# Kernel tuning notes

Hardware: AMD Instinct MI355X
Metric: run time of the kernel (lower is better)

## Reference

```python
import jax, jax.numpy as jnp
import numpy as np

HIDDEN = 2048
HEADS = 16
HEAD_DIM = HIDDEN // HEADS  # 128
THETA = 10000.0


def _rope_cache(seq_len, dim, theta=THETA):
    inv_freq = 1.0 / (theta ** (jnp.arange(0, dim, 2, dtype=jnp.float32) / dim))
    t = jnp.arange(seq_len, dtype=jnp.float32)
    freqs = jnp.outer(t, inv_freq)            # [S, dim/2]
    emb = jnp.concatenate([freqs, freqs], -1)  # [S, dim]
    return jnp.cos(emb), jnp.sin(emb)


def _rotate_half(x):
    x1, x2 = jnp.split(x, 2, axis=-1)
    return jnp.concatenate([-x2, x1], axis=-1)


def setup_inputs() -> dict:
    key = jax.random.key(0)
    ks = jax.random.split(key, 5)
    B, S = 2, 2048
    scale = 1.0 / np.sqrt(HIDDEN)
    return {
        "hidden_states": jax.random.normal(ks[0], (B, S, HIDDEN), jnp.float32),
        "wq": jax.random.normal(ks[1], (HIDDEN, HIDDEN), jnp.float32) * scale,
        "wk": jax.random.normal(ks[2], (HIDDEN, HIDDEN), jnp.float32) * scale,
        "wv": jax.random.normal(ks[3], (HIDDEN, HIDDEN), jnp.float32) * scale,
        "wo": jax.random.normal(ks[4], (HIDDEN, HIDDEN), jnp.float32) * scale,
    }


def reference(hidden_states, wq, wk, wv, wo):
    B, S, D = hidden_states.shape
    H, Hd = HEADS, HEAD_DIM
    # projections (nn.Linear: x @ W^T), reshape to [B, H, S, Hd]
    def proj(w):
        return (hidden_states @ w.T).reshape(B, S, H, Hd).transpose(0, 2, 1, 3)
    q, k, v = proj(wq), proj(wk), proj(wv)
    # RoPE
    cos, sin = _rope_cache(S, Hd)             # [S, Hd]
    q = q * cos + _rotate_half(q) * sin
    k = k * cos + _rotate_half(k) * sin
    # scaled dot-product attention with causal mask
    scores = jnp.einsum("bhqd,bhkd->bhqk", q, k) / jnp.sqrt(jnp.float32(Hd))
    causal = jnp.tril(jnp.ones((S, S), bool))
    scores = jnp.where(causal, scores, -jnp.inf)
    attn = jax.nn.softmax(scores, axis=-1)
    out = jnp.einsum("bhqk,bhkd->bhqd", attn, v)  # [B, H, S, Hd]
    out = out.transpose(0, 2, 1, 3).reshape(B, S, D)
    return out @ wo.T
```

## Files before the change

### kernel.cpp

```cpp
#include <hip/hip_runtime.h>
#include <hip/hip_bf16.h>

#define S_LEN  2048
#define BATCH  2
#define NH     16
#define HD     128
#define HIDDEN 2048
#define MROWS  (BATCH*S_LEN)

typedef __attribute__((ext_vector_type(8))) short bf16x8;
typedef __attribute__((ext_vector_type(4))) short s16x4;
typedef __attribute__((ext_vector_type(4))) float f32x4;

__device__ __forceinline__ float bf2f(short s) {
    union { float f; unsigned int u; } v;
    v.u = ((unsigned int)(unsigned short)s) << 16;
    return v.f;
}
__device__ __forceinline__ short f2bf(float f) {
    union { float f; unsigned int u; } v;
    v.f = f;
    unsigned int r = v.u + 0x7fffu + ((v.u >> 16) & 1u);
    return (short)(r >> 16);
}
__device__ __forceinline__ f32x4 mfma16(bf16x8 a, bf16x8 b, f32x4 c) {
    return __builtin_amdgcn_mfma_f32_16x16x32_bf16(a, b, c, 0, 0, 0);
}
__device__ __forceinline__ void gload16(const void* g, void* l) {
    __builtin_amdgcn_global_load_lds(
        (const __attribute__((address_space(1))) void*)g,
        (__attribute__((address_space(3))) void*)l, 16, 0, 0);
}

#define SEG (4194304)
__global__ void cast_k(const float* hs, const float* wq, const float* wk,
                       const float* wv, const float* wo, short* dst)
{
    size_t i = ((size_t)blockIdx.x * 256 + threadIdx.x) * 8;
    int seg = (int)(i >> 22);
    const float* s;
    size_t off;
    if (seg < 2)      { s = hs; off = i; }
    else if (seg == 2){ s = wq; off = i - 2 * (size_t)SEG; }
    else if (seg == 3){ s = wk; off = i - 3 * (size_t)SEG; }
    else if (seg == 4){ s = wv; off = i - 4 * (size_t)SEG; }
    else              { s = wo; off = i - 5 * (size_t)SEG; }
    f32x4 lo = *(const f32x4*)(s + off);
    f32x4 hi = *(const f32x4*)(s + off + 4);
    short v[8];
#pragma unroll
    for (int j = 0; j < 4; ++j) { v[j] = f2bf(lo[j]); v[4 + j] = f2bf(hi[j]); }
    *(bf16x8*)(dst + i) = *(bf16x8*)v;
}

template<int MODE>
__global__ __launch_bounds__(256, 4)
void gemm_bt(const short* A, const short* W0, const short* W1, const short* W2,
             short* Oq, short* Ok, short* Ov, float* Of)
{
    __shared__ short smem[2 * 128 * 64];
    short* As = smem;
    short* Bs = smem + 128 * 64;

    const int tid  = threadIdx.x;
    const int lane = tid & 63;
    const int wv   = tid >> 6;
    const int wr   = wv >> 1, wc = wv & 1;
    const int fr   = lane & 15, fg = lane >> 4;

    const int mt = blockIdx.x;
    int nt = blockIdx.y;
    const short* W = W0;
    short* Ob = Oq;
    int osel = 0;
    if (MODE == 0) {
        osel = nt >> 4; nt &= 15;
        W  = (osel == 0) ? W0 : (osel == 1) ? W1 : W2;
        Ob = (osel == 0) ? Oq : (osel == 1) ? Ok : Ov;
    }
    const int row0 = mt * 128, col0 = nt * 128;
    const int sr = tid >> 3, sb = tid & 7;

    f32x4 acc[4][4];
#pragma unroll
    for (int m = 0; m < 4; ++m)
#pragma unroll
        for (int n = 0; n < 4; ++n) acc[m][n] = (f32x4){0.f, 0.f, 0.f, 0.f};

    for (int k0 = 0; k0 < HIDDEN; k0 += 64) {
        __syncthreads();
#pragma unroll
        for (int it = 0; it < 4; ++it) {
            int r = it * 32 + sr;
            gload16(A + (size_t)(row0 + r) * HIDDEN + k0 + ((sb ^ (r & 7)) * 8),
                    (char*)As + (it * 256 + wv * 64) * 16);
        }
#pragma unroll
        for (int it = 0; it < 4; ++it) {
            int r = it * 32 + sr;
            gload16(W + (size_t)(col0 + r) * HIDDEN + k0 + ((sb ^ (r & 7)) * 8),
                    (char*)Bs + (it * 256 + wv * 64) * 16);
        }
        __syncthreads();
#pragma unroll
        for (int ks = 0; ks < 2; ++ks) {
            bf16x8 a[4], b[4];
#pragma unroll
            for (int m = 0; m < 4; ++m) {
                int r = wr * 64 + m * 16 + fr;
                a[m] = *(const bf16x8*)&As[r * 64 + (((ks * 4 + fg) ^ (r & 7)) * 8)];
            }
#pragma unroll
            for (int n = 0; n < 4; ++n) {
                int r = wc * 64 + n * 16 + fr;
                b[n] = *(const bf16x8*)&Bs[r * 64 + (((ks * 4 + fg) ^ (r & 7)) * 8)];
            }
#pragma unroll
            for (int m = 0; m < 4; ++m)
#pragma unroll
                for (int n = 0; n < 4; ++n)
                    acc[m][n] = mfma16(a[m], b[n], acc[m][n]);
        }
    }

    if (MODE == 0 && osel == 2) {
        __syncthreads();
#pragma unroll
        for (int m = 0; m < 4; ++m)
#pragma unroll
            for (int j = 0; j < 4; ++j) {
                int row = wr * 64 + m * 16 + fg * 4 + j;
#pragma unroll
                for (int n = 0; n < 4; ++n) {
                    int col = wc * 64 + n * 16 + fr;
                    smem[col * 128 + (((row >> 3) ^ (col & 15)) * 8) + (row & 7)] =
                        f2bf(acc[m][n][j]);
                }
            }
        __syncthreads();
        const int b_ = row0 >> 11;
        const int bh = b_ * NH + nt;
        const int s0 = row0 & (S_LEN - 1);
#pragma unroll
        for (int it = 0; it < 8; ++it) {
            int c = it * 256 + tid;
            int d = c >> 4, sbk = c & 15;
            bf16x8 vv = *(const bf16x8*)&smem[d * 128 + ((sbk ^ (d & 15)) * 8)];
            *(bf16x8*)(Ov + ((size_t)bh * HD + d) * S_LEN + s0 + sbk * 8) = vv;
        }
    } else {
#pragma unroll
        for (int m = 0; m < 4; ++m)
#pragma unroll
            for (int j = 0; j < 4; ++j) {
                int mrow = row0 + wr * 64 + m * 16 + fg * 4 + j;
#pragma unroll
                for (int n = 0; n < 4; ++n) {
                    int col = col0 + wc * 64 + n * 16 + fr;
                    float val = acc[m][n][j];
                    if (MODE == 0) {
                        int b_ = mrow >> 11, s = mrow & (S_LEN - 1);
                        int h = col >> 7, d = col & (HD - 1);
                        Ob[((size_t)(b_ * NH + h) * S_LEN + s) * HD + d] = f2bf(val);
                    } else {
                        Of[(size_t)mrow * HIDDEN + col] = val;
                    }
                }
            }
    }
}

__global__ void rope_table_k(float* tab)
{
    int i = blockIdx.x * 256 + threadIdx.x;
    if (i >= S_LEN * 64) return;
    int s = i >> 6, d = i & 63;
    float inv = 1.0f / powf(10000.0f, (float)d * (1.0f / 64.0f));
    float ang = (float)s * inv;
    tab[2 * i]     = cosf(ang);
    tab[2 * i + 1] = sinf(ang);
}

__global__ void rope_apply_k(short* Q, short* K, const float* tab)
{
    int i = blockIdx.x * 256 + threadIdx.x;
    int d8 = i & 7;
    int s  = (i >> 3) & (S_LEN - 1);
    int bh = i >> 14;
    size_t base = ((size_t)bh * S_LEN + s) * HD + d8 * 8;
    const float* tp = tab + (s * 64 + d8 * 8) * 2;
    f32x4 t[4];
#pragma unroll
    for (int j = 0; j < 4; ++j) t[j] = *(const f32x4*)(tp + j * 4);

    bf16x8 q1 = *(bf16x8*)(Q + base), q2 = *(bf16x8*)(Q + base + 64);
    bf16x8 k1 = *(bf16x8*)(K + base), k2 = *(bf16x8*)(K + base + 64);
    short oq1[8], oq2[8], ok1[8], ok2[8];
    const float qs = 0.08838834764831845f;
#pragma unroll
    for (int j = 0; j < 8; ++j) {
        float c  = t[j >> 1][(j & 1) * 2];
        float sn = t[j >> 1][(j & 1) * 2 + 1];
        float a1 = bf2f(q1[j]), a2 = bf2f(q2[j]);
        oq1[j] = f2bf((a1 * c - a2 * sn) * qs);
        oq2[j] = f2bf((a2 * c + a1 * sn) * qs);
        float b1 = bf2f(k1[j]), b2 = bf2f(k2[j]);
        ok1[j] = f2bf(b1 * c - b2 * sn);
        ok2[j] = f2bf(b2 * c + b1 * sn);
    }
    *(bf16x8*)(Q + base)      = *(bf16x8*)oq1;
    *(bf16x8*)(Q + base + 64) = *(bf16x8*)oq2;
    *(bf16x8*)(K + base)      = *(bf16x8*)ok1;
    *(bf16x8*)(K + base + 64) = *(bf16x8*)ok2;
}

__global__ __launch_bounds__(256, 2)
void attn_k(const short* Q, const short* K, const short* Vt, short* AO)
{
    __shared__ short Ks[2][64 * 128];
    __shared__ short Vs[2][128 * 64];

    const int tid = threadIdx.x, lane = tid & 63, wv = tid >> 6;
    const int fr = lane & 15, fg = lane >> 4;
    const int bid = blockIdx.x;
    const int bh   = bid & 31;
    const int sub  = bid >> 5;
    const int p    = sub >> 1;
    const int half = sub & 1;

    const short* Qb = Q  + (size_t)bh * S_LEN * HD;
    const short* Kb = K  + (size_t)bh * S_LEN * HD;
    const short* Vb = Vt + (size_t)bh * HD * S_LEN;
    const int b_ = bh >> 4, h = bh & 15;

#define SWK(r) (((r) & 3) | ((((r) >> 3) & 3) << 2))
#define STAGE(t, bufi)                                                          \
    do {                                                                        \
        const int kb_ = (t) * 64;                                               \
        _Pragma("unroll")                                                       \
        for (int i_ = 0; i_ < 4; ++i_) {                                        \
            int c_ = i_ * 256 + tid;                                            \
            int r_ = c_ >> 4, bb_ = c_ & 15;                                    \
            gload16(Kb + (size_t)(kb_ + r_) * HD + ((bb_ ^ SWK(r_)) * 8),       \
                    (char*)&Ks[bufi][0] + (i_ * 256 + wv * 64) * 16);           \
        }                                                                       \
        _Pragma("unroll")                                                       \
        for (int i_ = 0; i_ < 4; ++i_) {                                        \
            int c_ = i_ * 256 + tid;                                            \
            int r_ = c_ >> 3, bb_ = c_ & 7;                                     \
            gload16(Vb + (size_t)r_ * S_LEN + kb_ + ((bb_ ^ (r_ & 7)) * 8),     \
                    (char*)&Vs[bufi][0] + (i_ * 256 + wv * 64) * 16);           \
        }                                                                       \
    } while (0)

#pragma unroll 1
    for (int phase = 0; phase < 2; ++phase) {
        const int qt = phase ? (15 - p) : p;
        const int qbase = qt * 128 + half * 64 + wv * 16;

        bf16x8 qf[4];
#pragma unroll
        for (int ks = 0; ks < 4; ++ks)
            qf[ks] = *(const bf16x8*)(Qb + (size_t)(qbase + fr) * HD
                                      + ks * 32 + fg * 8);

        f32x4 oT[8];
#pragma unroll
        for (int nd = 0; nd < 8; ++nd) oT[nd] = (f32x4){0.f, 0.f, 0.f, 0.f};
        float mrun = -1e30f, lrun = 0.f;

        const int ntiles = qt * 2 + 1 + half;
        __syncthreads();
        STAGE(0, 0);

        for (int t = 0; t < ntiles; ++t) {
            const int buf = t & 1;
            __syncthreads();
            if (t + 1 < ntiles) STAGE(t + 1, buf ^ 1);
            const int kb = t * 64;

            if (kb <= qbase + 15) {
                f32x4 sc[4];
#pragma unroll
                for (int ni = 0; ni < 4; ++ni) sc[ni] = (f32x4){0.f, 0.f, 0.f, 0.f};
                __builtin_amdgcn_s_setprio(1);
#pragma unroll
                for (int ks = 0; ks < 4; ++ks) {
                    bf16x8 kf[4];
#pragma unroll
                    for (int ni = 0; ni < 4; ++ni) {
                        int rk = ((ni & 1) << 5) + ((fr >> 2) << 3)
                               + ((ni >> 1) << 2) + (fr & 3);
                        kf[ni] = *(const bf16x8*)&Ks[buf][rk * 128
                                     + (((ks * 4 + fg) ^ fr) * 8)];
                    }
#pragma unroll
                    for (int ni = 0; ni < 4; ++ni)
                        sc[ni] = mfma16(kf[ni], qf[ks], sc[ni]);
                }
                __builtin_amdgcn_s_setprio(0);
                const int qrow = qbase + fr;
                if (kb + 63 > qbase) {
#pragma unroll
                    for (int ni = 0; ni < 4; ++ni)
#pragma unroll
                        for (int j = 0; j < 4; ++j) {
                            int kcol = kb + ((ni & 1) << 5) + (fg << 3)
                                     + ((ni >> 1) << 2) + j;
                            if (kcol > qrow) sc[ni][j] = -1e30f;
                        }
                }
                float mx = sc[0][0];
#pragma unroll
                for (int ni = 0; ni < 4; ++ni)
#pragma unroll
                    for (int j = 0; j < 4; ++j) mx = fmaxf(mx, sc[ni][j]);
                mx = fmaxf(mx, __shfl_xor(mx, 16));
                mx = fmaxf(mx, __shfl_xor(mx, 32));
                if (mx > mrun) {
                    float scale = __expf(mrun - mx);
                    mrun = mx;
                    lrun *= scale;
#pragma unroll
                    for (int nd = 0; nd < 8; ++nd)
#pragma unroll
                        for (int j = 0; j < 4; ++j) oT[nd][j] *= scale;
                }
                float rs = 0.f;
                short pw[16];
#pragma unroll
                for (int ni = 0; ni < 4; ++ni)
#pragma unroll
                    for (int j = 0; j < 4; ++j) {
                        float pe = __expf(sc[ni][j] - mrun);
                        rs += pe;
                        pw[((ni & 1) << 3) + ((ni >> 1) << 2) + j] = f2bf(pe);
                    }
                bf16x8 pf0 = *(bf16x8*)&pw[0];
                bf16x8 pf1 = *(bf16x8*)&pw[8];
                rs += __shfl_xor(rs, 16);
                rs += __shfl_xor(rs, 32);
                lrun += rs;
                __builtin_amdgcn_s_setprio(1);
#pragma unroll
                for (int nd = 0; nd < 8; ++nd) {
                    const int d = nd * 16 + fr;
                    bf16x8 vf0 = *(const bf16x8*)&Vs[buf][d * 64 + ((fg ^ (d & 7)) * 8)];
                    bf16x8 vf1 = *(const bf16x8*)&Vs[buf][d * 64 + (((4 + fg) ^ (d & 7)) * 8)];
                    oT[nd] = mfma16(vf0, pf0, oT[nd]);
                    oT[nd] = mfma16(vf1, pf1, oT[nd]);
                }
                __builtin_amdgcn_s_setprio(0);
            }
        }

        float inv = 1.0f / lrun;
        int srow = qbase + fr;
#pragma unroll
        for (int nd = 0; nd < 8; ++nd) {
            s16x4 w;
#pragma unroll
            for (int j = 0; j < 4; ++j) w[j] = f2bf(oT[nd][j] * inv);
            *(s16x4*)(AO + ((size_t)b_ * S_LEN + srow) * HIDDEN
                      + h * HD + nd * 16 + fg * 4) = w;
        }
    }
#undef STAGE
#undef SWK
}

extern "C" void kernel_launch(void* const* d_in, const int* in_sizes, int n_in,
                              void* d_out, int out_size, void* d_ws, size_t ws_size,
                              hipStream_t stream)
{
    const float* hs = (const float*)d_in[0];
    const float* wq = (const float*)d_in[1];
    const float* wk = (const float*)d_in[2];
    const float* wvp = (const float*)d_in[3];
    const float* wo = (const float*)d_in[4];
    float* out = (float*)d_out;

    char* ws = (char*)d_ws;
    short* CB  = (short*)ws;
    short* Hb  = CB;
    short* Wqb = CB + 2 * (size_t)SEG;
    short* Wkb = CB + 3 * (size_t)SEG;
    short* Wvb = CB + 4 * (size_t)SEG;
    short* Wob = CB + 5 * (size_t)SEG;
    short* Qb  = (short*)(ws + 50331648);
    short* Kb  = (short*)(ws + 67108864);
    short* Vb  = (short*)(ws + 83886080);
    short* AO  = Hb;
    float* tab = (float*)(ws + 100663296);

    cast_k<<<dim3(12288), dim3(256), 0, stream>>>(hs, wq, wk, wvp, wo, CB);
    rope_table_k<<<dim3(512), dim3(256), 0, stream>>>(tab);
    gemm_bt<0><<<dim3(32, 48), dim3(256), 0, stream>>>(
        Hb, Wqb, Wkb, Wvb, Qb, Kb, Vb, nullptr);
    rope_apply_k<<<dim3(2048), dim3(256), 0, stream>>>(Qb, Kb, tab);
    attn_k<<<dim3(512), dim3(256), 0, stream>>>(Qb, Kb, Vb, AO);
    gemm_bt<1><<<dim3(32, 16), dim3(256), 0, stream>>>(
        AO, Wob, nullptr, nullptr, nullptr, nullptr, nullptr, out);
}
```

Measured before the change: 355.3 us.

## Rewrite projection GEMMs as 8-wave 256x128 tiles with 4-slot async LDS pipeline

Replaces the 4-wave 128x128 GEMM with a 512-thread kernel computing 256x128 tiles. It uses a 4-slot LDS ring of 32-wide K chunks, prefetching three stages ahead with global_load_lds. Explicit vmcnt/lgkmcnt waits, raw s_barrier and s_setprio are meant to overlap MFMA with loads and LDS reads, hiding memory latency that the single-buffered loop exposed. In exchange, grids get smaller (768 and 256 blocks, one block per CU), and hand-tuned waitcnt counts risk subtle races.

```diff
diff --git a/kernel.cpp b/kernel.cpp
--- a/kernel.cpp
+++ b/kernel.cpp
@@ -31,6 +31,9 @@
         (const __attribute__((address_space(1))) void*)g,
         (__attribute__((address_space(3))) void*)l, 16, 0, 0);
 }
+#define SBAR()  asm volatile("s_barrier" ::: "memory")
+#define LGKM0() do { asm volatile("s_waitcnt lgkmcnt(0)" ::: "memory"); \
+                     __builtin_amdgcn_sched_barrier(0); } while (0)
 
 #define SEG (4194304)
 __global__ void cast_k(const float* hs, const float* wq, const float* wk,
@@ -54,18 +57,16 @@
 }
 
 template<int MODE>
-__global__ __launch_bounds__(256, 4)
-void gemm_bt(const short* A, const short* W0, const short* W1, const short* W2,
-             short* Oq, short* Ok, short* Ov, float* Of)
-{
-    __shared__ short smem[2 * 128 * 64];
-    short* As = smem;
-    short* Bs = smem + 128 * 64;
+__global__ __launch_bounds__(512, 1)
+void gemm8p(const short* A, const short* W0, const short* W1, const short* W2,
+            short* Oq, short* Ok, short* Ov, float* Of)
+{
+    __shared__ short lds[49152];
 
     const int tid  = threadIdx.x;
     const int lane = tid & 63;
     const int wv   = tid >> 6;
-    const int wr   = wv >> 1, wc = wv & 1;
+    const int wr   = wv & 3, wc = wv >> 2;
     const int fr   = lane & 15, fg = lane >> 4;
 
     const int mt = blockIdx.x;
@@ -78,8 +79,43 @@
         W  = (osel == 0) ? W0 : (osel == 1) ? W1 : W2;
         Ob = (osel == 0) ? Oq : (osel == 1) ? Ok : Ov;
     }
-    const int row0 = mt * 128, col0 = nt * 128;
-    const int sr = tid >> 3, sb = tid & 7;
+    const int row0 = mt * 256, col0 = nt * 128;
+
+#define STAGEH(hh)                                                              \
+    do {                                                                        \
+        const int sl_ = (hh) & 3;                                               \
+        const int kg_ = (hh) * 32;                                              \
+        _Pragma("unroll")                                                       \
+        for (int it_ = 0; it_ < 2; ++it_) {                                     \
+            int c_ = it_ * 512 + tid;                                           \
+            int ln_ = c_ >> 3;                                                  \
+            int cr_ = (c_ & 7) ^ (ln_ & 7);                                     \
+            int sr_ = 2 * ln_ + (cr_ >> 2);                                     \
+            int sk_ = (cr_ & 3) * 8;                                            \
+            gload16(A + (size_t)(row0 + sr_) * HIDDEN + kg_ + sk_,              \
+                    (char*)lds + sl_ * 16384 + c_ * 16);                        \
+        }                                                                       \
+        {                                                                       \
+            int c_ = tid;                                                       \
+            int ln_ = c_ >> 3;                                                  \
+            int cr_ = (c_ & 7) ^ (ln_ & 7);                                     \
+            int sr_ = 2 * ln_ + (cr_ >> 2);                                     \
+            int sk_ = (cr_ & 3) * 8;                                            \
+            gload16(W + (size_t)(col0 + sr_) * HIDDEN + kg_ + sk_,              \
+                    (char*)lds + 65536 + sl_ * 8192 + c_ * 16);                 \
+        }                                                                       \
+    } while (0)
+
+    auto ldsA = [&](int sl, int r, int kc) -> bf16x8 {
+        int ln = r >> 1;
+        int cs = (((r & 1) << 2) + kc) ^ (ln & 7);
+        return *(const bf16x8*)((const char*)lds + sl * 16384 + ln * 128 + cs * 16);
+    };
+    auto ldsB = [&](int sl, int r, int kc) -> bf16x8 {
+        int ln = r >> 1;
+        int cs = (((r & 1) << 2) + kc) ^ (ln & 7);
+        return *(const bf16x8*)((const char*)lds + 65536 + sl * 8192 + ln * 128 + cs * 16);
+    };
 
     f32x4 acc[4][4];
 #pragma unroll
@@ -87,44 +123,54 @@
 #pragma unroll
         for (int n = 0; n < 4; ++n) acc[m][n] = (f32x4){0.f, 0.f, 0.f, 0.f};
 
-    for (int k0 = 0; k0 < HIDDEN; k0 += 64) {
-        __syncthreads();
-#pragma unroll
-        for (int it = 0; it < 4; ++it) {
-            int r = it * 32 + sr;
-            gload16(A + (size_t)(row0 + r) * HIDDEN + k0 + ((sb ^ (r & 7)) * 8),
-                    (char*)As + (it * 256 + wv * 64) * 16);
-        }
-#pragma unroll
-        for (int it = 0; it < 4; ++it) {
-            int r = it * 32 + sr;
-            gload16(W + (size_t)(col0 + r) * HIDDEN + k0 + ((sb ^ (r & 7)) * 8),
-                    (char*)Bs + (it * 256 + wv * 64) * 16);
-        }
-        __syncthreads();
-#pragma unroll
-        for (int ks = 0; ks < 2; ++ks) {
-            bf16x8 a[4], b[4];
-#pragma unroll
-            for (int m = 0; m < 4; ++m) {
-                int r = wr * 64 + m * 16 + fr;
-                a[m] = *(const bf16x8*)&As[r * 64 + (((ks * 4 + fg) ^ (r & 7)) * 8)];
-            }
-#pragma unroll
-            for (int n = 0; n < 4; ++n) {
-                int r = wc * 64 + n * 16 + fr;
-                b[n] = *(const bf16x8*)&Bs[r * 64 + (((ks * 4 + fg) ^ (r & 7)) * 8)];
-            }
-#pragma unroll
-            for (int m = 0; m < 4; ++m)
-#pragma unroll
-                for (int n = 0; n < 4; ++n)
-                    acc[m][n] = mfma16(a[m], b[n], acc[m][n]);
-        }
+    STAGEH(0); STAGEH(1); STAGEH(2);
+    asm volatile("s_waitcnt vmcnt(6)" ::: "memory");
+    SBAR();
+
+#pragma unroll 1
+    for (int h = 0; h < 64; ++h) {
+        const int sl = h & 3;
+        bf16x8 b0 = ldsB(sl, wc * 64 +  0 + fr, fg);
+        bf16x8 b1 = ldsB(sl, wc * 64 + 16 + fr, fg);
+        bf16x8 b2 = ldsB(sl, wc * 64 + 32 + fr, fg);
+        bf16x8 b3 = ldsB(sl, wc * 64 + 48 + fr, fg);
+        bf16x8 a0 = ldsA(sl, wr * 64 +  0 + fr, fg);
+        bf16x8 a1 = ldsA(sl, wr * 64 + 16 + fr, fg);
+        if (h + 3 < 64) STAGEH(h + 3);
+        SBAR();
+        LGKM0();
+        __builtin_amdgcn_s_setprio(1);
+        acc[0][0] = mfma16(a0, b0, acc[0][0]);
+        acc[0][1] = mfma16(a0, b1, acc[0][1]);
+        acc[0][2] = mfma16(a0, b2, acc[0][2]);
+        acc[0][3] = mfma16(a0, b3, acc[0][3]);
+        acc[1][0] = mfma16(a1, b0, acc[1][0]);
+        acc[1][1] = mfma16(a1, b1, acc[1][1]);
+        acc[1][2] = mfma16(a1, b2, acc[1][2]);
+        acc[1][3] = mfma16(a1, b3, acc[1][3]);
+        __builtin_amdgcn_s_setprio(0);
+        SBAR();
+        bf16x8 a2 = ldsA(sl, wr * 64 + 32 + fr, fg);
+        bf16x8 a3 = ldsA(sl, wr * 64 + 48 + fr, fg);
+        SBAR();
+        LGKM0();
+        __builtin_amdgcn_s_setprio(1);
+        acc[2][0] = mfma16(a2, b0, acc[2][0]);
+        acc[2][1] = mfma16(a2, b1, acc[2][1]);
+        acc[2][2] = mfma16(a2, b2, acc[2][2]);
+        acc[2][3] = mfma16(a2, b3, acc[2][3]);
+        acc[3][0] = mfma16(a3, b0, acc[3][0]);
+        acc[3][1] = mfma16(a3, b1, acc[3][1]);
+        acc[3][2] = mfma16(a3, b2, acc[3][2]);
+        acc[3][3] = mfma16(a3, b3, acc[3][3]);
+        __builtin_amdgcn_s_setprio(0);
+        if (h < 61) asm volatile("s_waitcnt vmcnt(6)" ::: "memory");
+        else        asm volatile("s_waitcnt vmcnt(0)" ::: "memory");
+        SBAR();
     }
+#undef STAGEH
 
     if (MODE == 0 && osel == 2) {
-        __syncthreads();
 #pragma unroll
         for (int m = 0; m < 4; ++m)
 #pragma unroll
@@ -133,7 +179,7 @@
 #pragma unroll
                 for (int n = 0; n < 4; ++n) {
                     int col = wc * 64 + n * 16 + fr;
-                    smem[col * 128 + (((row >> 3) ^ (col & 15)) * 8) + (row & 7)] =
+                    lds[col * 256 + (((row >> 3) ^ (col & 31)) * 8) + (row & 7)] =
                         f2bf(acc[m][n][j]);
                 }
             }
@@ -143,10 +189,10 @@
         const int s0 = row0 & (S_LEN - 1);
 #pragma unroll
         for (int it = 0; it < 8; ++it) {
-            int c = it * 256 + tid;
-            int d = c >> 4, sbk = c & 15;
-            bf16x8 vv = *(const bf16x8*)&smem[d * 128 + ((sbk ^ (d & 15)) * 8)];
-            *(bf16x8*)(Ov + ((size_t)bh * HD + d) * S_LEN + s0 + sbk * 8) = vv;
+            int c = it * 512 + tid;
+            int d = c >> 5, sc = c & 31;
+            bf16x8 vv = *(const bf16x8*)&lds[d * 256 + ((sc ^ (d & 31)) * 8)];
+            *(bf16x8*)(Ov + ((size_t)bh * HD + d) * S_LEN + s0 + sc * 8) = vv;
         }
     } else {
 #pragma unroll
@@ -160,8 +206,8 @@
                     float val = acc[m][n][j];
                     if (MODE == 0) {
                         int b_ = mrow >> 11, s = mrow & (S_LEN - 1);
-                        int h = col >> 7, d = col & (HD - 1);
-                        Ob[((size_t)(b_ * NH + h) * S_LEN + s) * HD + d] = f2bf(val);
+                        int h_ = col >> 7, d = col & (HD - 1);
+                        Ob[((size_t)(b_ * NH + h_) * S_LEN + s) * HD + d] = f2bf(val);
                     } else {
                         Of[(size_t)mrow * HIDDEN + col] = val;
                     }
@@ -395,10 +441,10 @@
 
     cast_k<<<dim3(12288), dim3(256), 0, stream>>>(hs, wq, wk, wvp, wo, CB);
     rope_table_k<<<dim3(512), dim3(256), 0, stream>>>(tab);
-    gemm_bt<0><<<dim3(32, 48), dim3(256), 0, stream>>>(
+    gemm8p<0><<<dim3(16, 48), dim3(512), 0, stream>>>(
         Hb, Wqb, Wkb, Wvb, Qb, Kb, Vb, nullptr);
     rope_apply_k<<<dim3(2048), dim3(256), 0, stream>>>(Qb, Kb, tab);
     attn_k<<<dim3(512), dim3(256), 0, stream>>>(Qb, Kb, Vb, AO);
-    gemm_bt<1><<<dim3(32, 16), dim3(256), 0, stream>>>(
+    gemm8p<1><<<dim3(16, 16), dim3(512), 0, stream>>>(
         AO, Wob, nullptr, nullptr, nullptr, nullptr, nullptr, out);
 }
```

Measured after the change: 366.5 us. +3.2%, slower.

## Fuse RoPE and query scaling into the QKV projection GEMM epilogue

Applied to the files above, without the earlier changes.

Removes the separate rope_apply kernel and applies rotary embedding plus the 1/sqrt(d) query scale directly in the QKV GEMM epilogue. The B-tile column mapping of each wave is remapped so that every thread holds both halves (d and d+64) of a rotation pair in registers. This saves a full read-modify-write pass over Q and K and one kernel launch. In exchange the epilogue does extra table loads and scalar bf16 stores.

```diff
diff --git a/kernel.cpp b/kernel.cpp
--- a/kernel.cpp
+++ b/kernel.cpp
@@ -53,10 +53,21 @@
     *(bf16x8*)(dst + i) = *(bf16x8*)v;
 }
 
+__global__ void rope_table_k(float* tab)
+{
+    int i = blockIdx.x * 256 + threadIdx.x;
+    if (i >= S_LEN * 64) return;
+    int s = i >> 6, d = i & 63;
+    float inv = 1.0f / powf(10000.0f, (float)d * (1.0f / 64.0f));
+    float ang = (float)s * inv;
+    tab[2 * i]     = cosf(ang);
+    tab[2 * i + 1] = sinf(ang);
+}
+
 template<int MODE>
 __global__ __launch_bounds__(256, 4)
 void gemm_bt(const short* A, const short* W0, const short* W1, const short* W2,
-             short* Oq, short* Ok, short* Ov, float* Of)
+             short* Oq, short* Ok, short* Ov, float* Of, const float* tab)
 {
     __shared__ short smem[2 * 128 * 64];
     short* As = smem;
@@ -112,7 +123,7 @@
             }
 #pragma unroll
             for (int n = 0; n < 4; ++n) {
-                int r = wc * 64 + n * 16 + fr;
+                int r = ((n & 1) << 6) + ((n >> 1) << 5) + wc * 16 + fr;
                 b[n] = *(const bf16x8*)&Bs[r * 64 + (((ks * 4 + fg) ^ (r & 7)) * 8)];
             }
 #pragma unroll
@@ -132,7 +143,7 @@
                 int row = wr * 64 + m * 16 + fg * 4 + j;
 #pragma unroll
                 for (int n = 0; n < 4; ++n) {
-                    int col = wc * 64 + n * 16 + fr;
+                    int col = ((n & 1) << 6) + ((n >> 1) << 5) + wc * 16 + fr;
                     smem[col * 128 + (((row >> 3) ^ (col & 15)) * 8) + (row & 7)] =
                         f2bf(acc[m][n][j]);
                 }
@@ -148,70 +159,40 @@
             bf16x8 vv = *(const bf16x8*)&smem[d * 128 + ((sbk ^ (d & 15)) * 8)];
             *(bf16x8*)(Ov + ((size_t)bh * HD + d) * S_LEN + s0 + sbk * 8) = vv;
         }
-    } else {
+    } else if (MODE == 0) {
+        const float sc_ = (osel == 0) ? 0.08838834764831845f : 1.0f;
+        const int d0 = wc * 16 + fr;
 #pragma unroll
         for (int m = 0; m < 4; ++m)
 #pragma unroll
             for (int j = 0; j < 4; ++j) {
                 int mrow = row0 + wr * 64 + m * 16 + fg * 4 + j;
+                int s = mrow & (S_LEN - 1), b_ = mrow >> 11;
+                const float* t0 = tab + ((s << 6) + d0) * 2;
+                const float* t1 = tab + ((s << 6) + 32 + d0) * 2;
+                float c0 = t0[0], n0 = t0[1];
+                float c1 = t1[0], n1 = t1[1];
+                float x0 = acc[m][0][j], y0 = acc[m][1][j];
+                float x1 = acc[m][2][j], y1 = acc[m][3][j];
+                size_t base = ((size_t)(b_ * NH + nt) * S_LEN + s) * HD;
+                Ob[base + d0]      = f2bf((x0 * c0 - y0 * n0) * sc_);
+                Ob[base + d0 + 64] = f2bf((y0 * c0 + x0 * n0) * sc_);
+                Ob[base + d0 + 32] = f2bf((x1 * c1 - y1 * n1) * sc_);
+                Ob[base + d0 + 96] = f2bf((y1 * c1 + x1 * n1) * sc_);
+            }
+    } else {
+#pragma unroll
+        for (int m = 0; m < 4; ++m)
+#pragma unroll
+            for (int j = 0; j < 4; ++j) {
+                int mrow = row0 + wr * 64 + m * 16 + fg * 4 + j;
 #pragma unroll
                 for (int n = 0; n < 4; ++n) {
-                    int col = col0 + wc * 64 + n * 16 + fr;
-                    float val = acc[m][n][j];
-                    if (MODE == 0) {
-                        int b_ = mrow >> 11, s = mrow & (S_LEN - 1);
-                        int h = col >> 7, d = col & (HD - 1);
-                        Ob[((size_t)(b_ * NH + h) * S_LEN + s) * HD + d] = f2bf(val);
-                    } else {
-                        Of[(size_t)mrow * HIDDEN + col] = val;
-                    }
+                    int col = col0 + ((n & 1) << 6) + ((n >> 1) << 5) + wc * 16 + fr;
+                    Of[(size_t)mrow * HIDDEN + col] = acc[m][n][j];
                 }
             }
     }
-}
-
-__global__ void rope_table_k(float* tab)
-{
-    int i = blockIdx.x * 256 + threadIdx.x;
-    if (i >= S_LEN * 64) return;
-    int s = i >> 6, d = i & 63;
-    float inv = 1.0f / powf(10000.0f, (float)d * (1.0f / 64.0f));
-    float ang = (float)s * inv;
-    tab[2 * i]     = cosf(ang);
-    tab[2 * i + 1] = sinf(ang);
-}
-
-__global__ void rope_apply_k(short* Q, short* K, const float* tab)
-{
-    int i = blockIdx.x * 256 + threadIdx.x;
-    int d8 = i & 7;
-    int s  = (i >> 3) & (S_LEN - 1);
-    int bh = i >> 14;
-    size_t base = ((size_t)bh * S_LEN + s) * HD + d8 * 8;
-    const float* tp = tab + (s * 64 + d8 * 8) * 2;
-    f32x4 t[4];
-#pragma unroll
-    for (int j = 0; j < 4; ++j) t[j] = *(const f32x4*)(tp + j * 4);
-
-    bf16x8 q1 = *(bf16x8*)(Q + base), q2 = *(bf16x8*)(Q + base + 64);
-    bf16x8 k1 = *(bf16x8*)(K + base), k2 = *(bf16x8*)(K + base + 64);
-    short oq1[8], oq2[8], ok1[8], ok2[8];
-    const float qs = 0.08838834764831845f;
-#pragma unroll
-    for (int j = 0; j < 8; ++j) {
-        float c  = t[j >> 1][(j & 1) * 2];
-        float sn = t[j >> 1][(j & 1) * 2 + 1];
-        float a1 = bf2f(q1[j]), a2 = bf2f(q2[j]);
-        oq1[j] = f2bf((a1 * c - a2 * sn) * qs);
-        oq2[j] = f2bf((a2 * c + a1 * sn) * qs);
-        float b1 = bf2f(k1[j]), b2 = bf2f(k2[j]);
-        ok1[j] = f2bf(b1 * c - b2 * sn);
-        ok2[j] = f2bf(b2 * c + b1 * sn);
-    }
-    *(bf16x8*)(Q + base)      = *(bf16x8*)oq1;
-    *(bf16x8*)(Q + base + 64) = *(bf16x8*)oq2;
-    *(bf16x8*)(K + base)      = *(bf16x8*)ok1;
-    *(bf16x8*)(K + base + 64) = *(bf16x8*)ok2;
 }
 
 __global__ __launch_bounds__(256, 2)
@@ -396,9 +377,8 @@
     cast_k<<<dim3(12288), dim3(256), 0, stream>>>(hs, wq, wk, wvp, wo, CB);
     rope_table_k<<<dim3(512), dim3(256), 0, stream>>>(tab);
     gemm_bt<0><<<dim3(32, 48), dim3(256), 0, stream>>>(
-        Hb, Wqb, Wkb, Wvb, Qb, Kb, Vb, nullptr);
-    rope_apply_k<<<dim3(2048), dim3(256), 0, stream>>>(Qb, Kb, tab);
+        Hb, Wqb, Wkb, Wvb, Qb, Kb, Vb, nullptr, tab);
     attn_k<<<dim3(512), dim3(256), 0, stream>>>(Qb, Kb, Vb, AO);
     gemm_bt<1><<<dim3(32, 16), dim3(256), 0, stream>>>(
-        AO, Wob, nullptr, nullptr, nullptr, nullptr, nullptr, out);
-}
+        AO, Wob, nullptr, nullptr, nullptr, nullptr, nullptr, out, nullptr);
+}
```

New measurement: 343.8 us. 3.2% less time.
